# Optimization experiments

Hardware: AMD Instinct MI355X
Metric: run time of the kernel (lower is better)

The kernel has to match this reference:

```python
import jax, jax.numpy as jnp
import numpy as np

STRICT_MAXIMA_BONUS = 10.0  # init kwarg strict_maxima_bonus


def _pad_rep(x):
    # replicate-pad spatial dims (D,H,W) by 1, matching kornia F.pad(..., 'replicate')
    return jnp.pad(x, ((0, 0), (0, 0), (1, 1), (1, 1), (1, 1)), mode='edge')


def _grad1(x):
    # kornia spatial_gradient3d(order=1, mode='diff'): central differences /2
    p = _pad_rep(x)
    c, l, r = slice(1, -1), slice(0, -2), slice(2, None)
    dx = 0.5 * (p[..., c, c, r] - p[..., c, c, l])  # d/dx along W
    dy = 0.5 * (p[..., c, r, c] - p[..., c, l, c])  # d/dy along H
    ds = 0.5 * (p[..., r, c, c] - p[..., l, c, c])  # d/ds along D
    return jnp.stack([dx, dy, ds], axis=-1)  # (B,C,D,H,W,3)


def _grad2(x):
    # kornia spatial_gradient3d(order=2, mode='diff'): channel order dxx,dyy,dss,dxy,dys,dxs
    p = _pad_rep(x)
    c, l, r = slice(1, -1), slice(0, -2), slice(2, None)
    dxx = p[..., c, c, l] + p[..., c, c, r] - 2.0 * x
    dyy = p[..., c, l, c] + p[..., c, r, c] - 2.0 * x
    dss = p[..., l, c, c] + p[..., r, c, c] - 2.0 * x
    dxy = p[..., c, l, l] + p[..., c, r, r] - p[..., c, r, l] - p[..., c, l, r]
    dys = p[..., l, l, c] + p[..., r, r, c] - p[..., r, l, c] - p[..., l, r, c]
    dxs = p[..., l, c, l] + p[..., r, c, r] - p[..., r, c, l] - p[..., l, c, r]
    return dxx, dyy, dss, dxy, dys, dxs


def _nms3d_mask(x):
    # kornia nms3d: x == maxpool3d(x, 3, stride 1, pad 1) (pad value -inf)
    mx = jax.lax.reduce_window(x, -jnp.inf, jax.lax.max,
                               (1, 1, 3, 3, 3), (1, 1, 1, 1, 1),
                               [(0, 0), (0, 0), (1, 1), (1, 1), (1, 1)])
    return x == mx


def _forward(x):
    B, C, D, H, W = x.shape
    b = _grad1(x)  # (B,C,D,H,W,3) order [dx,dy,ds]
    dxx, dyy, dss, dxy, dys, dxs = _grad2(x)
    dxy, dys, dxs = 0.25 * dxy, 0.25 * dys, 0.25 * dxs
    Hes = jnp.stack([dxx, dxy, dxs,
                     dxy, dyy, dys,
                     dxs, dys, dss], axis=-1).reshape(B, C, D, H, W, 3, 3)
    nms = _nms3d_mask(x)  # (B,C,D,H,W) bool
    # safe_solve_with_mask: LU solve valid where factorization succeeded (non-singular)
    det = jnp.linalg.det(Hes)
    solved = det != 0.0
    eye3 = jnp.eye(3, dtype=x.dtype)
    safe_H = jnp.where(solved[..., None, None], Hes, eye3)
    sol = jnp.linalg.solve(safe_H, b[..., None])[..., 0]  # (B,C,D,H,W,3)
    new_nms = nms & solved  # nms_mask.masked_scatter(nms_mask, solved_correctly)
    x_solved = jnp.where(new_nms[..., None], sol, 0.0)
    dx = -x_solved
    # zero refinements with any |component| > 0.7
    big = jnp.max(jnp.abs(dx), axis=-1, keepdims=True) > 0.7
    dx = jnp.where(big, 0.0, dx)
    dy_val = 0.5 * jnp.sum(b * dx, axis=-1)  # 0.5 * b^T dx per voxel
    y_max = x + dy_val + STRICT_MAXIMA_BONUS * new_nms.astype(x.dtype)
    # dx.flip(1): component order [s,y,x]; then move comps to axis 2 -> (B,C,3,D,H,W)
    dx_res = jnp.moveaxis(dx[..., ::-1], -1, 2)
    # kornia create_meshgrid3d(...).permute(0,4,1,2,3): channel values (d, w, h)
    dd, hh, ww = jnp.meshgrid(jnp.arange(D), jnp.arange(H), jnp.arange(W), indexing='ij')
    grid = jnp.stack([dd, ww, hh], axis=0).astype(x.dtype)  # (3,D,H,W)
    coords_max = grid[None, None] + dx_res  # (B,C,3,D,H,W)
    return coords_max, y_max


def setup_inputs() -> dict:
    key = jax.random.key(0)
    x = jax.random.normal(key, (2, 1, 8, 512, 512), dtype=jnp.float32)
    return {"x": x}


def reference(x):
    return _forward(x)
```

## Files before the change

### kernel.cpp

```cpp
#include <hip/hip_runtime.h>

namespace {

constexpr int Dd = 8, Hh = 512, Ww = 512, Bb = 2;
constexpr int PLANE = Hh * Ww;
constexpr size_t COORDS_SZ = (size_t)Bb * 3 * Dd * PLANE;

__global__ __launch_bounds__(256, 4) void cqi_kernel(const float* __restrict__ x,
                                                     float* __restrict__ out) {
    const int lane = threadIdx.x & 63;
    const int gid  = (blockIdx.x << 2) | (threadIdx.x >> 6);
    const int h  = gid & (Hh - 1);
    const int bd = gid >> 9;
    const int b  = bd >> 3;
    const int d  = bd & 7;

    const float* pl[3];
    pl[0] = x + (size_t)(d > 0      ? bd - 1 : bd) * PLANE;
    pl[1] = x + (size_t)bd * PLANE;
    pl[2] = x + (size_t)(d < Dd - 1 ? bd + 1 : bd) * PLANE;
    const int rw[3] = { (h > 0      ? h - 1 : 0) * Ww,
                         h * Ww,
                        (h < Hh - 1 ? h + 1 : h) * Ww };

    const int w0 = lane << 3;

    float cr[10];
    float cm[10];
    float fyc[10];
    float fsc[10];
    float syy[8];
    float sss[8];
    float uys[8];

#pragma unroll
    for (int a = 0; a < 3; ++a) {
#pragma unroll
        for (int e = 0; e < 3; ++e) {
            const float* p = pl[a] + rw[e] + w0;
            const float4 q0 = *reinterpret_cast<const float4*>(p);
            const float4 q1 = *reinterpret_cast<const float4*>(p + 4);
            const float lh = __shfl_up(q1.w, 1);
            const float rh = __shfl_down(q0.x, 1);
            float w[10];
            w[0] = (lane == 0)  ? q0.x : lh;
            w[1] = q0.x; w[2] = q0.y; w[3] = q0.z; w[4] = q0.w;
            w[5] = q1.x; w[6] = q1.y; w[7] = q1.z; w[8] = q1.w;
            w[9] = (lane == 63) ? q1.w : rh;
#pragma unroll
            for (int k = 0; k < 10; ++k) {
                if (a == 0 && e == 0) cm[k] = w[k];
                else                  cm[k] = fmaxf(cm[k], w[k]);
                if (a == 1 && e == 1) cr[k] = w[k];
                if (a == 1 && e == 0) fyc[k] = w[k];
                if (a == 1 && e == 2) fyc[k] = w[k] - fyc[k];
                if (a == 0 && e == 1) fsc[k] = w[k];
                if (a == 2 && e == 1) fsc[k] = w[k] - fsc[k];
                if (k >= 1 && k <= 8) {
                    const int m = k - 1;
                    if (a == 1 && e == 0) syy[m] = w[k];
                    if (a == 1 && e == 2) syy[m] += w[k];
                    if (a == 0 && e == 1) sss[m] = w[k];
                    if (a == 2 && e == 1) sss[m] += w[k];
                    if (a == 0 && e == 0) uys[m] = w[k];
                    if (a == 0 && e == 2) uys[m] -= w[k];
                    if (a == 2 && e == 0) uys[m] -= w[k];
                    if (a == 2 && e == 2) uys[m] += w[k];
                }
            }
        }
    }

    float* coords = out;
    float* ymax   = out + COORDS_SZ;
    const size_t idx = (size_t)(h * Ww) + w0;
    const size_t cb  = ((size_t)(b * 3) * Dd + d) * PLANE + idx;
    const size_t yb  = (size_t)bd * PLANE + idx;
    const float df = (float)d, hf = (float)h, wf = (float)w0;

#pragma unroll
    for (int half = 0; half < 2; ++half) {
        float4 oc0, oc1, oc2, oy;
        float* oc0p = &oc0.x; float* oc1p = &oc1.x;
        float* oc2p = &oc2.x; float* oyp = &oy.x;
#pragma unroll
        for (int j = 0; j < 4; ++j) {
            const int i = half * 4 + j;
            const float c0 = cr[i + 1];

            const float fx = 0.5f * (cr[i + 2] - cr[i]);
            const float fy = 0.5f * fyc[i + 1];
            const float fs = 0.5f * fsc[i + 1];

            const float dxx = (cr[i] + cr[i + 2]) - 2.0f * c0;
            const float dyy = syy[i] - 2.0f * c0;
            const float dss = sss[i] - 2.0f * c0;
            const float dxy = 0.25f * (fyc[i + 2] - fyc[i]);
            const float dxs = 0.25f * (fsc[i + 2] - fsc[i]);
            const float dys = 0.25f * uys[i];

            const float mx = fmaxf(fmaxf(cm[i], cm[i + 1]), cm[i + 2]);
            const bool nms = (c0 == mx);

            const float A00 = dyy * dss - dys * dys;
            const float A01 = dys * dxs - dxy * dss;
            const float A02 = dxy * dys - dyy * dxs;
            const float det = dxx * A00 + dxy * A01 + dxs * A02;
            const bool solved = (det != 0.0f);

            const float A11 = dxx * dss - dxs * dxs;
            const float A12 = dxy * dxs - dxx * dys;
            const float A22 = dxx * dyy - dxy * dxy;
            const float ninv = -__builtin_amdgcn_rcpf(det);
            const float sx = (A00 * fx + A01 * fy + A02 * fs) * ninv;
            const float sy = (A01 * fx + A11 * fy + A12 * fs) * ninv;
            const float ss = (A02 * fx + A12 * fy + A22 * fs) * ninv;

            const bool newnms = nms && solved;
            float dxv = newnms ? sx : 0.0f;
            float dyv = newnms ? sy : 0.0f;
            float dsv = newnms ? ss : 0.0f;

            const float mabs = fmaxf(fabsf(dxv), fmaxf(fabsf(dyv), fabsf(dsv)));
            const bool keep = (mabs <= 0.7f);
            dxv = keep ? dxv : 0.0f;
            dyv = keep ? dyv : 0.0f;
            dsv = keep ? dsv : 0.0f;

            const float dyval = 0.5f * (fx * dxv + fy * dyv + fs * dsv);

            oyp[j]  = c0 + dyval + (newnms ? 10.0f : 0.0f);
            oc0p[j] = df + dsv;
            oc1p[j] = (wf + (float)i) + dyv;
            oc2p[j] = hf + dxv;
        }
        const size_t off = (size_t)(half * 4);
        *reinterpret_cast<float4*>(coords + cb + off)                          = oc0;
        *reinterpret_cast<float4*>(coords + cb + (size_t)Dd * PLANE + off)     = oc1;
        *reinterpret_cast<float4*>(coords + cb + (size_t)2 * Dd * PLANE + off) = oc2;
        *reinterpret_cast<float4*>(ymax + yb + off)                            = oy;
    }
}

}

extern "C" void kernel_launch(void* const* d_in, const int* in_sizes, int n_in,
                              void* d_out, int out_size, void* d_ws, size_t ws_size,
                              hipStream_t stream) {
    const float* x = (const float*)d_in[0];
    float* out = (float*)d_out;
    dim3 grid(Bb * Dd * Hh / 4, 1, 1);
    dim3 block(256, 1, 1);
    hipLaunchKernelGGL(cqi_kernel, grid, block, 0, stream, x, out);
}
```

Measured before the change: 86.77 us.

## Stage shared 3x6-row input tile in LDS for 4-row blocks

Each block now cooperatively loads the 18 input rows (3 depth planes by 6 rows) its 4 waves need into shared memory with coalesced float4 loads, then reads the 3x3 neighbourhood rows from LDS instead of global memory. Previously each wave issued 9 row loads, so each block read 36 rows, mostly redundantly through cache. This cuts global and L2 traffic but adds 36KB of LDS per block and a barrier, which may limit occupancy below the declared four blocks per CU.

After: 88.11 us. About the same (+1.5%).

```diff
diff --git a/kernel.cpp b/kernel.cpp
--- a/kernel.cpp
+++ b/kernel.cpp
@@ -8,22 +8,39 @@
 
 __global__ __launch_bounds__(256, 4) void cqi_kernel(const float* __restrict__ x,
                                                      float* __restrict__ out) {
+    __shared__ float lds[18 * Ww];
+
     const int lane = threadIdx.x & 63;
-    const int gid  = (blockIdx.x << 2) | (threadIdx.x >> 6);
-    const int h  = gid & (Hh - 1);
-    const int bd = gid >> 9;
+    const int wv   = threadIdx.x >> 6;
+    const int gid0 = blockIdx.x << 2;
+    const int h0 = gid0 & (Hh - 1);
+    const int bd = gid0 >> 9;
     const int b  = bd >> 3;
     const int d  = bd & 7;
 
-    const float* pl[3];
-    pl[0] = x + (size_t)(d > 0      ? bd - 1 : bd) * PLANE;
-    pl[1] = x + (size_t)bd * PLANE;
-    pl[2] = x + (size_t)(d < Dd - 1 ? bd + 1 : bd) * PLANE;
-    const int rw[3] = { (h > 0      ? h - 1 : 0) * Ww,
-                         h * Ww,
-                        (h < Hh - 1 ? h + 1 : h) * Ww };
+    float4 st[9];
+    int    lo[9];
+#pragma unroll
+    for (int u = 0; u < 9; ++u) {
+        const int s   = wv + (u << 2);
+        const int r   = s >> 1;
+        const int seg = s & 1;
+        const int a   = r / 6;
+        const int wr  = r - a * 6;
+        int pd = d + a - 1;  pd = pd < 0 ? 0 : (pd > Dd - 1 ? Dd - 1 : pd);
+        int sr = h0 - 1 + wr; sr = sr < 0 ? 0 : (sr > Hh - 1 ? Hh - 1 : sr);
+        const float* g = x + (size_t)(b * Dd + pd) * PLANE + sr * Ww
+                           + (seg << 8) + (lane << 2);
+        st[u] = *reinterpret_cast<const float4*>(g);
+        lo[u] = r * Ww + (seg << 8) + (lane << 2);
+    }
+#pragma unroll
+    for (int u = 0; u < 9; ++u)
+        *reinterpret_cast<float4*>(&lds[lo[u]]) = st[u];
+    __syncthreads();
 
     const int w0 = lane << 3;
+    const int h  = h0 + wv;
 
     float cr[10];
     float cm[10];
@@ -37,7 +54,7 @@
     for (int a = 0; a < 3; ++a) {
 #pragma unroll
         for (int e = 0; e < 3; ++e) {
-            const float* p = pl[a] + rw[e] + w0;
+            const float* p = &lds[(a * 6 + wv + e) * Ww + w0];
             const float4 q0 = *reinterpret_cast<const float4*>(p);
             const float4 q1 = *reinterpret_cast<const float4*>(p + 4);
             const float lh = __shfl_up(q1.w, 1);
```
